# Performance work log

Hardware: AMD Instinct MI355X
Metric: run time of the kernel (lower is better)

## Reference

```python
import jax, jax.numpy as jnp
import numpy as np

THRESH = 1.0
BETA = 0.95
NUM_STEPS = 10

# snnTorch Leaky default: heaviside spike with ATan surrogate grad (alpha=2 -> 1/(1+(pi*x)^2))
@jax.custom_vjp
def spike(x):
    return (x > 0).astype(x.dtype)

def _spike_fwd(x):
    return (x > 0).astype(x.dtype), x

def _spike_bwd(x, g):
    return (g / (1.0 + (jnp.pi * x) ** 2),)

spike.defvjp(_spike_fwd, _spike_bwd)

def conv2d_same(x, w, b):
    y = jax.lax.conv_general_dilated(
        x, w, window_strides=(1, 1), padding=[(1, 1), (1, 1)],
        dimension_numbers=('NCHW', 'OIHW', 'NCHW'))
    return y + b[None, :, None, None]

def maxpool2(x):
    return jax.lax.reduce_window(x, -jnp.inf, jax.lax.max,
                                 (1, 1, 2, 2), (1, 1, 2, 2), 'VALID')

def setup_inputs() -> dict:
    key = jax.random.key(0)
    ks = jax.random.split(key, 9)
    B = 512
    x = jax.random.normal(ks[0], (B, 3, 32, 32), dtype=jnp.float32)
    def u(k, shape, fan_in):
        bound = 1.0 / np.sqrt(fan_in)
        return jax.random.uniform(k, shape, jnp.float32, -bound, bound)
    conv1_w = u(ks[1], (32, 3, 3, 3), 3 * 9)
    conv1_b = u(ks[2], (32,), 3 * 9)
    conv2_w = u(ks[3], (64, 32, 3, 3), 32 * 9)
    conv2_b = u(ks[4], (64,), 32 * 9)
    fc1_w = u(ks[5], (1000, 4096), 4096)
    fc1_b = u(ks[6], (1000,), 4096)
    fc2_w = u(ks[7], (10, 1000), 1000)
    fc2_b = u(ks[8], (10,), 1000)
    return {'x': x, 'conv1_w': conv1_w, 'conv1_b': conv1_b,
            'conv2_w': conv2_w, 'conv2_b': conv2_b,
            'fc1_w': fc1_w, 'fc1_b': fc1_b, 'fc2_w': fc2_w, 'fc2_b': fc2_b}

def reference(x, conv1_w, conv1_b, conv2_w, conv2_b, fc1_w, fc1_b, fc2_w, fc2_b):
    h = jax.nn.relu(conv2d_same(x, conv1_w, conv1_b))
    h = maxpool2(h)                     # [B,32,16,16]
    h = jax.nn.relu(conv2d_same(h, conv2_w, conv2_b))
    h = maxpool2(h)                     # [B,64,8,8]
    h = h.reshape(h.shape[0], -1)       # [B,4096]
    cur1 = h @ fc1_w.T + fc1_b          # constant across timesteps (x is static)

    def step(carry, _):
        mem1, mem2 = carry
        # snnTorch Leaky: reset from PREVIOUS mem (detached), subtract-reset
        reset1 = jax.lax.stop_gradient(spike(mem1 - THRESH))
        mem1 = BETA * mem1 + cur1 - reset1 * THRESH
        spk1 = spike(mem1 - THRESH)
        cur2 = spk1 @ fc2_w.T + fc2_b
        reset2 = jax.lax.stop_gradient(spike(mem2 - THRESH))
        mem2 = BETA * mem2 + cur2 - reset2 * THRESH
        spk2 = spike(mem2 - THRESH)
        return (mem1, mem2), (spk2, mem2)

    mem1_0 = jnp.zeros_like(cur1)
    mem2_0 = jnp.zeros((cur1.shape[0], fc2_w.shape[0]), cur1.dtype)
    _, (spk2_rec, mem2_rec) = jax.lax.scan(step, (mem1_0, mem2_0), None, length=NUM_STEPS)
    return spk2_rec, mem2_rec
```

## Files before the change

### kernel.cpp

```cpp
#include <hip/hip_runtime.h>


__global__ void __launch_bounds__(256) conv2_wt(
    const float* __restrict__ w, float* __restrict__ wt) {
  int tid = blockIdx.x * 256 + threadIdx.x;
  if (tid >= 64 * 288) return;
  int i = tid & 15;
  int node = tid >> 4;
  int kk = node % 9;
  int gic = node / 9;
  int ic = gic & 31, g = gic >> 5;
  wt[tid] = w[(size_t)(g * 16 + i) * 288 + ic * 9 + kk];
}

__global__ void __launch_bounds__(256) conv1_pool(
    const float* __restrict__ x, const float* __restrict__ w,
    const float* __restrict__ bias, float* __restrict__ p1) {
  const int b = blockIdx.x;
  __shared__ float sx[3 * 34 * 34];
  const float* xb = x + (size_t)b * 3072;
  for (int i = threadIdx.x; i < 3 * 34 * 34; i += 256) sx[i] = 0.0f;
  __syncthreads();
  for (int i = threadIdx.x; i < 3072; i += 256) {
    int ic = i >> 10, y = (i >> 5) & 31, xx = i & 31;
    sx[ic * 1156 + (y + 1) * 34 + (xx + 1)] = xb[i];
  }
  __syncthreads();

  const int px = threadIdx.x & 15, py = threadIdx.x >> 4;
  float xr[3][4][4];
#pragma unroll
  for (int ic = 0; ic < 3; ic++)
#pragma unroll
    for (int r = 0; r < 4; r++)
#pragma unroll
      for (int c = 0; c < 4; c++)
        xr[ic][r][c] = sx[ic * 1156 + (2 * py + r) * 34 + (2 * px + c)];

  float* outp = p1 + (size_t)b * 8192 + py * 16 + px;
  for (int oc = 0; oc < 32; oc++) {
    const float* wo = w + oc * 27;
    float a0 = 0.0f, a1 = 0.0f, a2 = 0.0f, a3 = 0.0f;
#pragma unroll
    for (int ky = 0; ky < 3; ky++)
#pragma unroll
      for (int kx = 0; kx < 3; kx++)
#pragma unroll
        for (int ic = 0; ic < 3; ic++) {
          float wv = wo[ic * 9 + ky * 3 + kx];
          a0 = fmaf(wv, xr[ic][ky][kx], a0);
          a1 = fmaf(wv, xr[ic][ky][kx + 1], a1);
          a2 = fmaf(wv, xr[ic][ky + 1][kx], a2);
          a3 = fmaf(wv, xr[ic][ky + 1][kx + 1], a3);
        }
    float bv = bias[oc];
    a0 = fmaxf(__fadd_rn(a0, bv), 0.0f);
    a1 = fmaxf(__fadd_rn(a1, bv), 0.0f);
    a2 = fmaxf(__fadd_rn(a2, bv), 0.0f);
    a3 = fmaxf(__fadd_rn(a3, bv), 0.0f);
    outp[oc * 256] = fmaxf(fmaxf(a0, a1), fmaxf(a2, a3));
  }
}

__global__ void __launch_bounds__(256) conv2_pool(
    const float* __restrict__ p1, const float* __restrict__ wt,
    const float* __restrict__ bias, float* __restrict__ p2) {
  const int b = blockIdx.x;
  __shared__ float sx[32 * 18 * 18];
  const float* xb = p1 + (size_t)b * 8192;
  for (int i = threadIdx.x; i < 32 * 18 * 18; i += 256) sx[i] = 0.0f;
  __syncthreads();
  for (int i = threadIdx.x; i < 8192; i += 256) {
    int ic = i >> 8, y = (i >> 4) & 15, xx = i & 15;
    sx[ic * 324 + (y + 1) * 18 + (xx + 1)] = xb[i];
  }
  __syncthreads();

  const int t = threadIdx.x;
  const int px = t & 7, py = (t >> 3) & 7;
  const int g = __builtin_amdgcn_readfirstlane(t >> 6);
  const float* wg = wt + (size_t)g * 32 * 9 * 16;

  float acc[16][4];
#pragma unroll
  for (int i = 0; i < 16; i++)
    acc[i][0] = acc[i][1] = acc[i][2] = acc[i][3] = 0.0f;

#pragma unroll
  for (int ky = 0; ky < 3; ky++) {
#pragma unroll
    for (int kx = 0; kx < 3; kx++) {
      const int r0 = (2 * py + ky) * 18 + 2 * px + kx;
      const int r1 = r0 + 18;
#pragma unroll 4
      for (int ic = 0; ic < 32; ic++) {
        float x00 = sx[ic * 324 + r0];
        float x01 = sx[ic * 324 + r0 + 1];
        float x10 = sx[ic * 324 + r1];
        float x11 = sx[ic * 324 + r1 + 1];
        const float* wp = wg + (size_t)(ic * 9 + ky * 3 + kx) * 16;
#pragma unroll
        for (int i = 0; i < 16; i++) {
          float wv = wp[i];
          acc[i][0] = fmaf(wv, x00, acc[i][0]);
          acc[i][1] = fmaf(wv, x01, acc[i][1]);
          acc[i][2] = fmaf(wv, x10, acc[i][2]);
          acc[i][3] = fmaf(wv, x11, acc[i][3]);
        }
      }
    }
  }

  float* outb = p2 + (size_t)b * 4096;
#pragma unroll
  for (int i = 0; i < 16; i++) {
    float bv = bias[g * 16 + i];
    float a0 = fmaxf(__fadd_rn(acc[i][0], bv), 0.0f);
    float a1 = fmaxf(__fadd_rn(acc[i][1], bv), 0.0f);
    float a2 = fmaxf(__fadd_rn(acc[i][2], bv), 0.0f);
    float a3 = fmaxf(__fadd_rn(acc[i][3], bv), 0.0f);
    outb[(g * 16 + i) * 64 + py * 8 + px] = fmaxf(fmaxf(a0, a1), fmaxf(a2, a3));
  }
}

__global__ void __launch_bounds__(256) fc1_panel(
    const float* __restrict__ A,
    const float* __restrict__ W,
    float* __restrict__ part) {
  __shared__ __align__(16) float As[16][132];
  __shared__ __align__(16) float Bs[16][68];
  const int t = threadIdx.x;
  const int m0 = blockIdx.x * 128, n0 = blockIdx.y * 64;
  const int z = blockIdx.z;
  const int k0 = z * 288;
  const int L = (z == 14) ? 64 : 288;

  const int lmA = t >> 1, lkA = (t & 1) * 8;
  const int lmB = t >> 2, lkB = (t & 3) * 4;
  const int nr = n0 + lmB;
  const float* Ap = A + (size_t)(m0 + lmA) * 4096 + k0 + lkA;
  const float* Bp = W + (size_t)(nr < 1000 ? nr : 0) * 4096 + k0 + lkB;
  const int tx = t & 15, ty = t >> 4;

  float acc[8][4];
#pragma unroll
  for (int i = 0; i < 8; i++)
#pragma unroll
    for (int j = 0; j < 4; j++) acc[i][j] = 0.0f;

  for (int kk = 0; kk < L; kk += 16) {
    float4 a0 = *(const float4*)Ap;
    float4 a1 = *(const float4*)(Ap + 4);
    float4 b4 = *(const float4*)Bp;
    As[lkA + 0][lmA] = a0.x; As[lkA + 1][lmA] = a0.y;
    As[lkA + 2][lmA] = a0.z; As[lkA + 3][lmA] = a0.w;
    As[lkA + 4][lmA] = a1.x; As[lkA + 5][lmA] = a1.y;
    As[lkA + 6][lmA] = a1.z; As[lkA + 7][lmA] = a1.w;
    Bs[lkB + 0][lmB] = b4.x; Bs[lkB + 1][lmB] = b4.y;
    Bs[lkB + 2][lmB] = b4.z; Bs[lkB + 3][lmB] = b4.w;
    __syncthreads();
#pragma unroll
    for (int k = 0; k < 16; k++) {
      float4 av0 = *(const float4*)&As[k][tx * 8];
      float4 av1 = *(const float4*)&As[k][tx * 8 + 4];
      float4 bv = *(const float4*)&Bs[k][ty * 4];
      float am[8] = {av0.x, av0.y, av0.z, av0.w, av1.x, av1.y, av1.z, av1.w};
#pragma unroll
      for (int i = 0; i < 8; i++) {
        acc[i][0] = fmaf(am[i], bv.x, acc[i][0]);
        acc[i][1] = fmaf(am[i], bv.y, acc[i][1]);
        acc[i][2] = fmaf(am[i], bv.z, acc[i][2]);
        acc[i][3] = fmaf(am[i], bv.w, acc[i][3]);
      }
    }
    __syncthreads();
    Ap += 16; Bp += 16;
  }

  float* pp = part + (size_t)z * 512000;
#pragma unroll
  for (int i = 0; i < 8; i++) {
    const int m = m0 + tx * 8 + i;
#pragma unroll
    for (int j = 0; j < 4; j++) {
      const int n = n0 + ty * 4 + j;
      if (n < 1000) pp[(size_t)m * 1000 + n] = acc[i][j];
    }
  }
}

__global__ void __launch_bounds__(256) snn_loop(
    const float* __restrict__ part,
    const float* __restrict__ fc1_b,
    const float* __restrict__ fc2_w,
    const float* __restrict__ fc2_b,
    float* __restrict__ out) {
  const int b = blockIdx.x;
  const int t = threadIdx.x;
  __shared__ float pw[40 * 289];
  __shared__ float spkp[4 * 289];

  for (int i = t; i < 40 * 289; i += 256) {
    int chain = i / 289, ii = i - chain * 289;
    int o = chain % 10, c = chain / 10;
    int len = (c == 3) ? 136 : 288;
    pw[i] = (ii < len) ? fc2_w[o * 1000 + c * 288 + ii] : 0.0f;
  }

  float cur1[4], mem1[4];
#pragma unroll
  for (int q = 0; q < 4; q++) {
    int j = t + q * 256;
    float c = 0.0f;
    if (j < 1000) {
      const float* pb = part + (size_t)b * 1000 + j;
      float tot = pb[0];
#pragma unroll
      for (int p = 1; p < 15; p++)
        tot = __fadd_rn(tot, pb[(size_t)p * 512000]);
      c = __fadd_rn(tot, fc1_b[j]);
    }
    cur1[q] = c;
    mem1[q] = 0.0f;
  }
  float m2 = 0.0f;
  __syncthreads();

  const int o4 = t % 10, c4 = t / 10;
  const float* wch = &pw[(c4 * 10 + o4) * 289];
  const float* sch = &spkp[c4 * 289];

  for (int s = 0; s < 10; s++) {
#pragma unroll
    for (int q = 0; q < 4; q++) {
      int j = t + q * 256;
      float m = mem1[q];
      float reset = (m > 1.0f) ? 1.0f : 0.0f;
      float t1 = __fmul_rn(0.95f, m);
      float t2 = __fadd_rn(t1, cur1[q]);
      m = __fsub_rn(t2, reset);
      mem1[q] = m;
      if (j < 1000) {
        int pc = (j >= 864) ? 3 : ((j >= 576) ? 2 : ((j >= 288) ? 1 : 0));
        spkp[pc * 289 + (j - pc * 288)] = (m > 1.0f) ? 1.0f : 0.0f;
      }
    }
    __syncthreads();

    float acc = 0.0f;
    if (t < 40) {
      if (c4 < 3) {
#pragma unroll 16
        for (int i = 0; i < 288; i++) acc = fmaf(sch[i], wch[i], acc);
      } else {
#pragma unroll 17
        for (int i = 0; i < 136; i++) acc = fmaf(sch[i], wch[i], acc);
      }
    }

    if (t < 64) {
      float p0 = __shfl(acc, o4, 64);
      float p1 = __shfl(acc, 10 + o4, 64);
      float p2 = __shfl(acc, 20 + o4, 64);
      float p3 = __shfl(acc, 30 + o4, 64);
      if (t < 10) {
        float tot = p0;
        tot = __fadd_rn(tot, p1);
        tot = __fadd_rn(tot, p2);
        tot = __fadd_rn(tot, p3);
        float c2 = __fadd_rn(tot, fc2_b[t]);
        float r2 = (m2 > 1.0f) ? 1.0f : 0.0f;
        float u1 = __fmul_rn(0.95f, m2);
        float u2 = __fadd_rn(u1, c2);
        m2 = __fsub_rn(u2, r2);
        out[s * 5120 + b * 10 + t] = (m2 > 1.0f) ? 1.0f : 0.0f;
        out[51200 + s * 5120 + b * 10 + t] = m2;
      }
    }
    __syncthreads();
  }
}

extern "C" void kernel_launch(void* const* d_in, const int* in_sizes, int n_in,
                              void* d_out, int out_size, void* d_ws,
                              size_t ws_size, hipStream_t stream) {
  const float* x   = (const float*)d_in[0];
  const float* c1w = (const float*)d_in[1];
  const float* c1b = (const float*)d_in[2];
  const float* c2w = (const float*)d_in[3];
  const float* c2b = (const float*)d_in[4];
  const float* f1w = (const float*)d_in[5];
  const float* f1b = (const float*)d_in[6];
  const float* f2w = (const float*)d_in[7];
  const float* f2b = (const float*)d_in[8];
  float* out = (float*)d_out;

  char* ws = (char*)d_ws;
  float* part = (float*)(ws);
  float* p1   = (float*)(ws);
  float* h    = (float*)(ws + (size_t)15 * 512 * 1000 * 4);
  float* wt   = (float*)(ws + (size_t)15 * 512 * 1000 * 4 + (size_t)512 * 4096 * 4);

  conv2_wt<<<72, 256, 0, stream>>>(c2w, wt);
  conv1_pool<<<512, 256, 0, stream>>>(x, c1w, c1b, p1);
  conv2_pool<<<512, 256, 0, stream>>>(p1, wt, c2b, h);
  fc1_panel<<<dim3(4, 16, 15), 256, 0, stream>>>(h, f1w, part);
  snn_loop<<<512, 256, 0, stream>>>(part, f1b, f2w, f2b, out);
}
```

Before: 267.4 us.

## Restructure fc1 GEMM with transposed activations, wave-uniform A loads, double-buffered B

Adds a kernel that transposes the conv output h into hT (K-major). The fc1 panel kernel is retiled to 64x128 blocks. Each wave reads its 16 batch rows directly from hT using wave-uniform (scalar-broadcast) loads instead of staging A through shared memory. The B tile is double-buffered in LDS with a register prefetch, which cuts one barrier per step. This trades an extra transpose pass and a larger workspace for fewer LDS writes and syncs, and relies on the cache to serve the uniform A loads.

```diff
diff --git a/kernel.cpp b/kernel.cpp
--- a/kernel.cpp
+++ b/kernel.cpp
@@ -11,6 +11,29 @@
   int gic = node / 9;
   int ic = gic & 31, g = gic >> 5;
   wt[tid] = w[(size_t)(g * 16 + i) * 288 + ic * 9 + kk];
+}
+
+__global__ void __launch_bounds__(256) transpose_h(
+    const float* __restrict__ h, float* __restrict__ hT) {
+  __shared__ float tile[64][65];
+  const int b0 = blockIdx.x * 64, c0 = blockIdx.y * 64;
+  const int tx = threadIdx.x & 15, ty = threadIdx.x >> 4;
+#pragma unroll
+  for (int i = 0; i < 4; i++) {
+    int b = ty + i * 16;
+    float4 v = *(const float4*)&h[(size_t)(b0 + b) * 4096 + c0 + tx * 4];
+    tile[b][tx * 4 + 0] = v.x; tile[b][tx * 4 + 1] = v.y;
+    tile[b][tx * 4 + 2] = v.z; tile[b][tx * 4 + 3] = v.w;
+  }
+  __syncthreads();
+#pragma unroll
+  for (int i = 0; i < 4; i++) {
+    int c = ty + i * 16;
+    float4 v;
+    v.x = tile[tx * 4 + 0][c]; v.y = tile[tx * 4 + 1][c];
+    v.z = tile[tx * 4 + 2][c]; v.w = tile[tx * 4 + 3][c];
+    *(float4*)&hT[(size_t)(c0 + c) * 512 + b0 + tx * 4] = v;
+  }
 }
 
 __global__ void __launch_bounds__(256) conv1_pool(
@@ -124,67 +147,79 @@
 }
 
 __global__ void __launch_bounds__(256) fc1_panel(
-    const float* __restrict__ A,
+    const float* __restrict__ hT,
     const float* __restrict__ W,
     float* __restrict__ part) {
-  __shared__ __align__(16) float As[16][132];
-  __shared__ __align__(16) float Bs[16][68];
+  __shared__ __align__(16) float Bs[2][16][128];
   const int t = threadIdx.x;
-  const int m0 = blockIdx.x * 128, n0 = blockIdx.y * 64;
+  const int m0 = blockIdx.x * 64, n0 = blockIdx.y * 128;
   const int z = blockIdx.z;
   const int k0 = z * 288;
   const int L = (z == 14) ? 64 : 288;
 
-  const int lmA = t >> 1, lkA = (t & 1) * 8;
-  const int lmB = t >> 2, lkB = (t & 3) * 4;
-  const int nr = n0 + lmB;
-  const float* Ap = A + (size_t)(m0 + lmA) * 4096 + k0 + lkA;
-  const float* Bp = W + (size_t)(nr < 1000 ? nr : 0) * 4096 + k0 + lkB;
-  const int tx = t & 15, ty = t >> 4;
-
-  float acc[8][4];
-#pragma unroll
-  for (int i = 0; i < 8; i++)
-#pragma unroll
-    for (int j = 0; j < 4; j++) acc[i][j] = 0.0f;
-
-  for (int kk = 0; kk < L; kk += 16) {
-    float4 a0 = *(const float4*)Ap;
-    float4 a1 = *(const float4*)(Ap + 4);
-    float4 b4 = *(const float4*)Bp;
-    As[lkA + 0][lmA] = a0.x; As[lkA + 1][lmA] = a0.y;
-    As[lkA + 2][lmA] = a0.z; As[lkA + 3][lmA] = a0.w;
-    As[lkA + 4][lmA] = a1.x; As[lkA + 5][lmA] = a1.y;
-    As[lkA + 6][lmA] = a1.z; As[lkA + 7][lmA] = a1.w;
-    Bs[lkB + 0][lmB] = b4.x; Bs[lkB + 1][lmB] = b4.y;
-    Bs[lkB + 2][lmB] = b4.z; Bs[lkB + 3][lmB] = b4.w;
+  const int w = __builtin_amdgcn_readfirstlane(t >> 6);
+  const int lane = t & 63;
+  const int mw = m0 + 16 * w;
+
+  const int ln = t >> 1, lk = (t & 1) * 8;
+  const int nrow = n0 + ln;
+  const float* Bp = W + (size_t)(nrow < 1000 ? nrow : 0) * 4096 + k0 + lk;
+
+  float acc[16][2];
+#pragma unroll
+  for (int j = 0; j < 16; j++) { acc[j][0] = 0.0f; acc[j][1] = 0.0f; }
+
+  {
+    float4 b0 = *(const float4*)Bp;
+    float4 b1 = *(const float4*)(Bp + 4);
+    Bs[0][lk + 0][ln] = b0.x; Bs[0][lk + 1][ln] = b0.y;
+    Bs[0][lk + 2][ln] = b0.z; Bs[0][lk + 3][ln] = b0.w;
+    Bs[0][lk + 4][ln] = b1.x; Bs[0][lk + 5][ln] = b1.y;
+    Bs[0][lk + 6][ln] = b1.z; Bs[0][lk + 7][ln] = b1.w;
+    Bp += 16;
+  }
+  __syncthreads();
+
+  const int nsteps = L / 16;
+  for (int step = 0; step < nsteps; step++) {
+    const int cur = step & 1, nxt = cur ^ 1;
+    float4 b0, b1;
+    const bool more = (step + 1 < nsteps);
+    if (more) {
+      b0 = *(const float4*)Bp;
+      b1 = *(const float4*)(Bp + 4);
+      Bp += 16;
+    }
+
+    const float* aT = hT + (size_t)(k0 + step * 16) * 512 + mw;
+#pragma unroll
+    for (int k = 0; k < 16; k++) {
+      const float* arow = aT + (size_t)k * 512;
+      float2 bv = *(const float2*)&Bs[cur][k][2 * lane];
+#pragma unroll
+      for (int j = 0; j < 16; j++) {
+        float a = arow[j];
+        acc[j][0] = fmaf(a, bv.x, acc[j][0]);
+        acc[j][1] = fmaf(a, bv.y, acc[j][1]);
+      }
+    }
+
+    if (more) {
+      Bs[nxt][lk + 0][ln] = b0.x; Bs[nxt][lk + 1][ln] = b0.y;
+      Bs[nxt][lk + 2][ln] = b0.z; Bs[nxt][lk + 3][ln] = b0.w;
+      Bs[nxt][lk + 4][ln] = b1.x; Bs[nxt][lk + 5][ln] = b1.y;
+      Bs[nxt][lk + 6][ln] = b1.z; Bs[nxt][lk + 7][ln] = b1.w;
+    }
     __syncthreads();
-#pragma unroll
-    for (int k = 0; k < 16; k++) {
-      float4 av0 = *(const float4*)&As[k][tx * 8];
-      float4 av1 = *(const float4*)&As[k][tx * 8 + 4];
-      float4 bv = *(const float4*)&Bs[k][ty * 4];
-      float am[8] = {av0.x, av0.y, av0.z, av0.w, av1.x, av1.y, av1.z, av1.w};
-#pragma unroll
-      for (int i = 0; i < 8; i++) {
-        acc[i][0] = fmaf(am[i], bv.x, acc[i][0]);
-        acc[i][1] = fmaf(am[i], bv.y, acc[i][1]);
-        acc[i][2] = fmaf(am[i], bv.z, acc[i][2]);
-        acc[i][3] = fmaf(am[i], bv.w, acc[i][3]);
-      }
-    }
-    __syncthreads();
-    Ap += 16; Bp += 16;
   }
 
   float* pp = part + (size_t)z * 512000;
-#pragma unroll
-  for (int i = 0; i < 8; i++) {
-    const int m = m0 + tx * 8 + i;
-#pragma unroll
-    for (int j = 0; j < 4; j++) {
-      const int n = n0 + ty * 4 + j;
-      if (n < 1000) pp[(size_t)m * 1000 + n] = acc[i][j];
+  const int n = n0 + 2 * lane;
+  if (n < 1000) {
+#pragma unroll
+    for (int j = 0; j < 16; j++) {
+      float2 v; v.x = acc[j][0]; v.y = acc[j][1];
+      *(float2*)&pp[(size_t)(mw + j) * 1000 + n] = v;
     }
   }
 }
@@ -296,14 +331,18 @@
   float* out = (float*)d_out;
 
   char* ws = (char*)d_ws;
+  const size_t PART_B = (size_t)15 * 512 * 1000 * 4;
+  const size_t H_B    = (size_t)512 * 4096 * 4;
   float* part = (float*)(ws);
   float* p1   = (float*)(ws);
-  float* h    = (float*)(ws + (size_t)15 * 512 * 1000 * 4);
-  float* wt   = (float*)(ws + (size_t)15 * 512 * 1000 * 4 + (size_t)512 * 4096 * 4);
+  float* h    = (float*)(ws + PART_B);
+  float* hT   = (float*)(ws + PART_B + H_B);
+  float* wt   = (float*)(ws + PART_B + 2 * H_B);
 
   conv2_wt<<<72, 256, 0, stream>>>(c2w, wt);
   conv1_pool<<<512, 256, 0, stream>>>(x, c1w, c1b, p1);
   conv2_pool<<<512, 256, 0, stream>>>(p1, wt, c2b, h);
-  fc1_panel<<<dim3(4, 16, 15), 256, 0, stream>>>(h, f1w, part);
+  transpose_h<<<dim3(8, 64), 256, 0, stream>>>(h, hT);
+  fc1_panel<<<dim3(8, 8, 15), 256, 0, stream>>>(hT, f1w, part);
   snn_loop<<<512, 256, 0, stream>>>(part, f1b, f2w, f2b, out);
 }
```

Result: slower. 345.4 us (+29.2%).
